# Kernel optimization log

Hardware: AMD Instinct MI355X
Metric: run time of the kernel (lower is better)

Reference implementation:

```python
import jax, jax.numpy as jnp
import numpy as np

# Config / sizes
N = 20000       # nodes
E = 320000      # edges (avg degree 16)
IN_DIM = 6      # node feature dim
PE = 8          # laplacian PE dims
ED = 4          # edge feature dim
H = 128         # hidden dim
OUT = 4         # output dim
L = 3           # message-passing layers
T = 3           # node types (typed encoders/decoders)


def mlp(z, W1, b1, W2, b2):
    # _make_mlp: Linear -> ReLU -> Linear
    return jax.nn.relu(z @ W1 + b1) @ W2 + b2


def typed_mlp(z, W1, b1, W2, b2, types):
    # W1: [T, Din, H]; compute all T branches, select per-node by type
    h = jax.nn.relu(jnp.einsum('ni,tih->tnh', z, W1) + b1[:, None, :])
    o = jnp.einsum('tnh,tho->tno', h, W2) + b2[:, None, :]
    onehot = jax.nn.one_hot(types, W1.shape[0], dtype=o.dtype)  # [N, T]
    return jnp.einsum('tno,nt->no', o, onehot)


def setup_inputs() -> dict:
    key = jax.random.key(0)
    ks = jax.random.split(key, 40)

    def w(k, shape, fan_in):
        return jax.random.normal(k, shape, dtype=jnp.float32) / np.float32(np.sqrt(fan_in))

    inp = {}
    inp['x'] = jax.random.normal(ks[0], (N, IN_DIM), dtype=jnp.float32)
    inp['pe'] = jax.random.normal(ks[1], (N, PE), dtype=jnp.float32)
    inp['edge_attr'] = jax.random.normal(ks[2], (E, ED), dtype=jnp.float32)
    # typed node encoders: (in_dim+pe_dims) -> H -> H
    inp['enc_W1'] = w(ks[3], (T, IN_DIM + PE, H), IN_DIM + PE)
    inp['enc_b1'] = jnp.zeros((T, H), jnp.float32)
    inp['enc_W2'] = w(ks[4], (T, H, H), H)
    inp['enc_b2'] = jnp.zeros((T, H), jnp.float32)
    # edge encoder: ED -> H -> H
    inp['ee_W1'] = w(ks[5], (ED, H), ED)
    inp['ee_b1'] = jnp.zeros((H,), jnp.float32)
    inp['ee_W2'] = w(ks[6], (H, H), H)
    inp['ee_b2'] = jnp.zeros((H,), jnp.float32)
    # per-layer edge update (3H->H->H), node update (2H->H->H), fusion (H->H->H)
    inp['eu_W1'] = w(ks[7], (L, 3 * H, H), 3 * H)
    inp['eu_b1'] = jnp.zeros((L, H), jnp.float32)
    inp['eu_W2'] = w(ks[8], (L, H, H), H)
    inp['eu_b2'] = jnp.zeros((L, H), jnp.float32)
    inp['nu_W1'] = w(ks[9], (L, 2 * H, H), 2 * H)
    inp['nu_b1'] = jnp.zeros((L, H), jnp.float32)
    inp['nu_W2'] = w(ks[10], (L, H, H), H)
    inp['nu_b2'] = jnp.zeros((L, H), jnp.float32)
    inp['fu_W1'] = w(ks[11], (L, H, H), H)
    inp['fu_b1'] = jnp.zeros((L, H), jnp.float32)
    inp['fu_W2'] = w(ks[12], (L, H, H), H)
    inp['fu_b2'] = jnp.zeros((L, H), jnp.float32)
    # typed decoders: H -> H -> OUT
    inp['dec_W1'] = w(ks[13], (T, H, H), H)
    inp['dec_b1'] = jnp.zeros((T, H), jnp.float32)
    inp['dec_W2'] = w(ks[14], (T, H, OUT), H)
    inp['dec_b2'] = jnp.zeros((T, OUT), jnp.float32)
    # int inputs
    inp['edge_index'] = jax.random.randint(ks[15], (2, E), 0, N)
    inp['node_types'] = jax.random.randint(ks[16], (N,), 0, T)
    return inp


def reference(x, pe, edge_attr,
              enc_W1, enc_b1, enc_W2, enc_b2,
              ee_W1, ee_b1, ee_W2, ee_b2,
              eu_W1, eu_b1, eu_W2, eu_b2,
              nu_W1, nu_b1, nu_W2, nu_b2,
              fu_W1, fu_b1, fu_W2, fu_b2,
              dec_W1, dec_b1, dec_W2, dec_b2,
              edge_index, node_types):
    n = x.shape[0]
    src, dst = edge_index[0], edge_index[1]
    # typed node encode on [x || pe]
    h_nodes = typed_mlp(jnp.concatenate([x, pe], axis=-1),
                        enc_W1, enc_b1, enc_W2, enc_b2, node_types)
    # edge encode
    h_edges = mlp(edge_attr, ee_W1, ee_b1, ee_W2, ee_b2)
    num_layers = eu_W1.shape[0]
    for l in range(num_layers):
        # gather endpoint states, edge MLP, residual on edges
        m_edge = mlp(jnp.concatenate([h_nodes[src], h_nodes[dst], h_edges], axis=-1),
                     eu_W1[l], eu_b1[l], eu_W2[l], eu_b2[l])
        h_edges = h_edges + m_edge
        # scatter-add aggregation to destination nodes (index_add_)
        m_node = jax.ops.segment_sum(h_edges, dst, num_segments=n)
        # node update + residual, then fusion (dropout is eval/identity)
        upd = mlp(jnp.concatenate([h_nodes, m_node], axis=-1),
                  nu_W1[l], nu_b1[l], nu_W2[l], nu_b2[l])
        local = h_nodes + upd
        h_nodes = mlp(local, fu_W1[l], fu_b1[l], fu_W2[l], fu_b2[l])
    # typed decode
    out = typed_mlp(h_nodes, dec_W1, dec_b1, dec_W2, dec_b2, node_types)
    return out
```

## Files before the change

### kernel.cpp

```cpp
#include <hip/hip_runtime.h>
#include <hip/hip_bf16.h>

typedef __hip_bfloat16 bf16;
typedef __attribute__((ext_vector_type(8))) short short8;
typedef __attribute__((ext_vector_type(4))) float floatx4;

#define HDIM 128
#define NCANON 27

__device__ __forceinline__ float b2f(bf16 v) { return __bfloat162float(v); }
__device__ __forceinline__ float s2f(short s) {
  return __uint_as_float(((unsigned int)(unsigned short)s) << 16);
}
__device__ __forceinline__ short f2s(float f) {
  return (short)__bfloat16_as_ushort(__float2bfloat16(f));
}

struct CanonDesc {
  const void* src[NCANON];
  int prefix[NCANON + 1];
};

__global__ void canon_kernel(CanonDesc d, const unsigned short* __restrict__ xraw,
                             int* __restrict__ flagOut, bf16* __restrict__ out, int total,
// ... 79 lines not shown
  }
}

__global__ void scan1_kernel(const int* __restrict__ cnt, int* __restrict__ bsum, int n) {
  int tid = threadIdx.x, lane = tid & 63, wave = tid >> 6;
  int i = blockIdx.x * 256 + tid;
  int v = (i < n) ? cnt[i] : 0;
  #pragma unroll
  for (int d = 32; d; d >>= 1) v += __shfl_down(v, d);
  __shared__ int ws[4];
  if (lane == 0) ws[wave] = v;
  __syncthreads();
  if (tid == 0) bsum[blockIdx.x] = ws[0] + ws[1] + ws[2] + ws[3];
}

__global__ void scan2_kernel(int* __restrict__ bsum, int nb) {
  int lane = threadIdx.x;
  int a0 = (lane < nb) ? bsum[lane] : 0;
  int b0 = (64 + lane < nb) ? bsum[64 + lane] : 0;
  int a = a0, b = b0;
  #pragma unroll
  for (int d = 1; d < 64; d <<= 1) { int t = __shfl_up(a, d); if (lane >= d) a += t; }
  int totA = __shfl(a, 63);
  #pragma unroll
  for (int d = 1; d < 64; d <<= 1) { int t = __shfl_up(b, d); if (lane >= d) b += t; }
  int totB = __shfl(b, 63);
  if (lane < nb) bsum[lane] = a - a0;
  if (64 + lane < nb) bsum[64 + lane] = b - b0 + totA;
  if (lane == 0) bsum[nb] = totA + totB;
}

__global__ void scan3_kernel(const int* __restrict__ cnt, const int* __restrict__ bsum,
                             int* __restrict__ row_start, int n, int nb) {
  __shared__ int sh[256];
  int tid = threadIdx.x;
  int i = blockIdx.x * 256 + tid;
  int v = (i < n) ? cnt[i] : 0;
  sh[tid] = v;
  __syncthreads();
  #pragma unroll
  for (int off = 1; off < 256; off <<= 1) {
    int t = (tid >= off) ? sh[tid - off] : 0;
    __syncthreads();
    sh[tid] += t;
    __syncthreads();
  }
  if (i < n) row_start[i] = bsum[blockIdx.x] + sh[tid] - v;
  if (blockIdx.x == 0 && tid == 0) row_start[n] = bsum[nb];
}

__global__ void scatter_kernel(const int* __restrict__ src, const int* __restrict__ dst,
                               const int* __restrict__ row_start, int* __restrict__ cursor,
                               const bf16* __restrict__ ea, bf16* __restrict__ eaS,
                               int* __restrict__ srcS, int* __restrict__ dstS, int E) {
  int e = blockIdx.x * 256 + threadIdx.x;
  if (e < E) {
    int d = dst[e];
    int pos = row_start[d] + atomicAdd(&cursor[d], 1);
    srcS[pos] = src[e];
    dstS[pos] = d;
    *(uint2*)(eaS + (size_t)pos * 4) = *(const uint2*)(ea + (size_t)e * 4);
  }
}

struct PackJob { const bf16* src; bf16* dst; int Ksrc; int KS; int srcCols; };
struct PackJobs { PackJob j[40]; };

__global__ void pack_all_kernel(PackJobs J) {
  PackJob job = J.j[blockIdx.y];
  int idx = blockIdx.x * 256 + threadIdx.x;
  int total = 8 * job.KS * 64;
  if (idx >= total) return;
  int lane = idx & 63;
  int ks = (idx >> 6) % job.KS;
  int ct = idx / (64 * job.KS);
  bf16* o = job.dst + (size_t)idx * 8;
  int ncol = ct * 16 + (lane & 15);
  int kb = ks * 32 + ((lane >> 4) & 3) * 8;
  #pragma unroll
  for (int jj = 0; jj < 8; jj++) {
    int k = kb + jj;
    o[jj] = (k < job.Ksrc && ncol < job.srcCols)
              ? job.src[(size_t)k * job.srcCols + ncol] : __float2bfloat16(0.f);
  }
}

__global__ void __launch_bounds__(256) ygemm_kernel(
    const bf16* __restrict__ X,
    const bf16* __restrict__ WpA, const bf16* __restrict__ WpB,
    bf16* __restrict__ outA, bf16* __restrict__ outB,
    float* __restrict__ mnode, int M) {
  const bf16* Wp = blockIdx.y ? WpB : WpA;
  bf16* outp = blockIdx.y ? outB : outA;
  constexpr int BM = 64, RT = 4, SK = 144;
  __shared__ bf16 Zt[BM * SK];
  const int tid = threadIdx.x;
  const int lane = tid & 63, wave = tid >> 6, colq = lane & 15, quad = lane >> 4;
  const int row0 = blockIdx.x * BM;
  if (blockIdx.y == 0) {
    float4 z = {0.f, 0.f, 0.f, 0.f};
    for (int i = tid; i < BM * 32; i += 256) {
      int row = i >> 5, q = i & 31;
      int gr = row0 + row;
      if (gr < M) *(float4*)(mnode + (size_t)gr * HDIM + q * 4) = z;
    }
  }
  {
    int row = tid >> 2, sub = tid & 3;
    int gr = row0 + row;
    bool ok = gr < M;
    #pragma unroll
    for (int j = 0; j < 4; j++) {
      int seg = j * 4 + sub;
      uint4 v = {0u, 0u, 0u, 0u};
      if (ok) v = *(const uint4*)(X + (size_t)gr * HDIM + seg * 8);
      *(uint4*)(&Zt[row * SK + seg * 8]) = v;
    }
  }
  __syncthreads();
  floatx4 acc[RT][2];
  #pragma unroll
  for (int rt = 0; rt < RT; rt++)
    #pragma unroll
    for (int c = 0; c < 2; c++) acc[rt][c] = (floatx4){0.f, 0.f, 0.f, 0.f};
  #pragma unroll
  for (int ks = 0; ks < 4; ks++) {
    short8 bfr0 = *(const short8*)(Wp + (((size_t)(wave * 2 + 0) * 4 + ks) * 64 + lane) * 8);
    short8 bfr1 = *(const short8*)(Wp + (((size_t)(wave * 2 + 1) * 4 + ks) * 64 + lane) * 8);
    #pragma unroll
    for (int rt = 0; rt < RT; rt++) {
      short8 a = *(const short8*)(&Zt[(rt * 16 + colq) * SK + ks * 32 + quad * 8]);
      acc[rt][0] = __builtin_amdgcn_mfma_f32_16x16x32_bf16(a, bfr0, acc[rt][0], 0, 0, 0);
      acc[rt][1] = __builtin_amdgcn_mfma_f32_16x16x32_bf16(a, bfr1, acc[rt][1], 0, 0, 0);
    }
  }
  __syncthreads();
  #pragma unroll
  for (int c = 0; c < 2; c++) {
    int col = wave * 32 + c * 16 + colq;
    #pragma unroll
    for (int rt = 0; rt < RT; rt++)
      #pragma unroll
      for (int r = 0; r < 4; r++)
        Zt[(rt * 16 + quad * 4 + r) * SK + col] = __float2bfloat16(acc[rt][c][r]);
  }
  __syncthreads();
  for (int i = tid; i < BM * 16; i += 256) {
    int row = i >> 4, seg = i & 15;
    int gr = row0 + row;
    if (gr < M)
      *(uint4*)(outp + (size_t)gr * HDIM + seg * 8) = *(const uint4*)(&Zt[row * SK + seg * 8]);
  }
}

template<bool WRITE_HE>
__global__ void __launch_bounds__(512) eu_kernel(
    const bf16* __restrict__ he, const bf16* __restrict__ ysrc, const bf16* __restrict__ ydst,
    const int* __restrict__ srcS, const int* __restrict__ dstS,
    const bf16* __restrict__ W1p, const bf16* __restrict__ b1v,
    const bf16* __restrict__ W2p, const bf16* __restrict__ b2v,
    bf16* __restrict__ outp, float* __restrict__ mnode, int M) {
  constexpr int BM = 64, RT = 4, SK = 272;
  __shared__ bf16 Zt[BM * SK];
  __shared__ int dstLds[BM];
  const int tid = threadIdx.x;
  const int lane = tid & 63, wave = tid >> 6, colq = lane & 15, quad = lane >> 4;
  const int nwg = gridDim.x, bid = blockIdx.x;
  const int qq = nwg >> 3, rr = nwg & 7;
  const int xcd = bid & 7, bidx = bid >> 3;
  const int blk = (xcd < rr ? xcd * (qq + 1) : rr * (qq + 1) + (xcd - rr) * qq) + bidx;
  const int row0 = blk * BM;
  {
    int row = tid >> 3, sub = tid & 7;
    int gr = row0 + row;
    bool ok = gr < M;
    int g0 = ok ? srcS[gr] : 0;
    int g1 = ok ? dstS[gr] : 0;
    if (sub == 0) dstLds[row] = ok ? g1 : -1;
    #pragma unroll
    for (int j = 0; j < 4; j++) {
      int c = j * 8 + sub;
      int part = c >> 4, seg = c & 15;
      if (part == 0) {
        short8 o = {0, 0, 0, 0, 0, 0, 0, 0};
        if (ok) {
          short8 a = *(const short8*)(ysrc + (size_t)g0 * HDIM + seg * 8);
          short8 b = *(const short8*)(ydst + (size_t)g1 * HDIM + seg * 8);
          #pragma unroll
          for (int k = 0; k < 8; k++) o[k] = f2s(s2f(a[k]) + s2f(b[k]));
        }
        *(short8*)(&Zt[row * SK + seg * 8]) = o;
      } else {
        uint4 v = {0u, 0u, 0u, 0u};
        if (ok) v = *(const uint4*)(he + (size_t)gr * HDIM + seg * 8);
        *(uint4*)(&Zt[row * SK + 128 + seg * 8]) = v;
      }
    }
  }
  __syncthreads();

  floatx4 acc[RT];
  #pragma unroll
  for (int rt = 0; rt < RT; rt++) acc[rt] = (floatx4){0.f, 0.f, 0.f, 0.f};
  #pragma unroll
  for (int ks = 0; ks < 4; ks++) {
    short8 bfr = *(const short8*)(W1p + (((size_t)wave * 4 + ks) * 64 + lane) * 8);
    #pragma unroll
    for (int rt = 0; rt < RT; rt++) {
      short8 a = *(const short8*)(&Zt[(rt * 16 + colq) * SK + 128 + ks * 32 + quad * 8]);
      acc[rt] = __builtin_amdgcn_mfma_f32_16x16x32_bf16(a, bfr, acc[rt], 0, 0, 0);
    }
  }
  {
    int col = wave * 16 + colq;
    float bv = b2f(b1v[col]);
    #pragma unroll
    for (int rt = 0; rt < RT; rt++)
      #pragma unroll
      for (int r = 0; r < 4; r++) {
        int lrow = rt * 16 + quad * 4 + r;
        float v = acc[rt][r] + bv + b2f(Zt[lrow * SK + col]);
        Zt[lrow * SK + col] = __float2bfloat16(fmaxf(v, 0.f));
      }
  }
  __syncthreads();

  #pragma unroll
  for (int rt = 0; rt < RT; rt++) acc[rt] = (floatx4){0.f, 0.f, 0.f, 0.f};
  #pragma unroll
  for (int ks = 0; ks < 4; ks++) {
    short8 bfr = *(const short8*)(W2p + (((size_t)wave * 4 + ks) * 64 + lane) * 8);
    #pragma unroll
    for (int rt = 0; rt < RT; rt++) {
      short8 a = *(const short8*)(&Zt[(rt * 16 + colq) * SK + ks * 32 + quad * 8]);
// ... 171 lines not shown
      #pragma unroll
      for (int r = 0; r < 4; r++)
        Zt[(wr * 32 + rt * 16 + quad * 4 + r) * SK + 128 + col] =
            __float2bfloat16(fmaxf(acc[rt][c][r] + bv, 0.f));
  }
  __syncthreads();

  #pragma unroll
  for (int rt = 0; rt < 2; rt++)
    #pragma unroll
    for (int c = 0; c < 2; c++) acc[rt][c] = (floatx4){0.f, 0.f, 0.f, 0.f};
  #pragma unroll
  for (int ks = 0; ks < 4; ks++) {
    short8 bfr0 = *(const short8*)(fuW2 + (((size_t)(wc * 2 + 0) * 4 + ks) * 64 + lane) * 8);
    short8 bfr1 = *(const short8*)(fuW2 + (((size_t)(wc * 2 + 1) * 4 + ks) * 64 + lane) * 8);
    #pragma unroll
    for (int rt = 0; rt < 2; rt++) {
      short8 a = *(const short8*)(&Zt[(wr * 32 + rt * 16 + colq) * SK + 128 + ks * 32 + quad * 8]);
      acc[rt][0] = __builtin_amdgcn_mfma_f32_16x16x32_bf16(a, bfr0, acc[rt][0], 0, 0, 0);
      acc[rt][1] = __builtin_amdgcn_mfma_f32_16x16x32_bf16(a, bfr1, acc[rt][1], 0, 0, 0);
    }
  }
  #pragma unroll
  for (int c = 0; c < 2; c++) {
    int col = wc * 32 + c * 16 + colq;
    float bv = b2f(fuB2[col]);
    #pragma unroll
    for (int rt = 0; rt < 2; rt++)
      #pragma unroll
      for (int r = 0; r < 4; r++) {
        int lrow = wr * 32 + rt * 16 + quad * 4 + r;
        Zt[lrow * SK + col] = __float2bfloat16(acc[rt][c][r] + bv);
      }
  }
  __syncthreads();
  for (int i = tid; i < BM * 16; i += 512) {
    int row = i >> 4, seg = i & 15;
    int gr = row0 + row;
    if (gr < M)
      *(uint4*)(outp + (size_t)gr * HDIM + seg * 8) = *(const uint4*)(&Zt[row * SK + seg * 8]);
  }
  if (!yW1a) return;

  #pragma unroll
  for (int which = 0; which < 2; which++) {
    const bf16* Wp = which ? yW1b : yW1a;
    bf16* outy = which ? ysB : ysA;
    #pragma unroll
    for (int rt = 0; rt < 2; rt++)
      #pragma unroll
      for (int c = 0; c < 2; c++) acc[rt][c] = (floatx4){0.f, 0.f, 0.f, 0.f};
    #pragma unroll
    for (int ks = 0; ks < 4; ks++) {
      short8 bfr0 = *(const short8*)(Wp + (((size_t)(wc * 2 + 0) * 4 + ks) * 64 + lane) * 8);
      short8 bfr1 = *(const short8*)(Wp + (((size_t)(wc * 2 + 1) * 4 + ks) * 64 + lane) * 8);
      #pragma unroll
      for (int rt = 0; rt < 2; rt++) {
        short8 a = *(const short8*)(&Zt[(wr * 32 + rt * 16 + colq) * SK + ks * 32 + quad * 8]);
        acc[rt][0] = __builtin_amdgcn_mfma_f32_16x16x32_bf16(a, bfr0, acc[rt][0], 0, 0, 0);
        acc[rt][1] = __builtin_amdgcn_mfma_f32_16x16x32_bf16(a, bfr1, acc[rt][1], 0, 0, 0);
      }
    }
    #pragma unroll
    for (int c = 0; c < 2; c++) {
      int col = wc * 32 + c * 16 + colq;
      #pragma unroll
      for (int rt = 0; rt < 2; rt++)
        #pragma unroll
        for (int r = 0; r < 4; r++)
          Zt[(wr * 32 + rt * 16 + quad * 4 + r) * SK + 128 + col] =
              __float2bfloat16(acc[rt][c][r]);
    }
    __syncthreads();
    for (int i = tid; i < BM * 16; i += 512) {
      int row = i >> 4, seg = i & 15;
      int gr = row0 + row;
      if (gr < M)
        *(uint4*)(outy + (size_t)gr * HDIM + seg * 8) = *(const uint4*)(&Zt[row * SK + 128 + seg * 8]);
    }
    __syncthreads();
  }
}

__global__ void __launch_bounds__(256) encee_kernel(
    int eeBlocks, int ngrid64,
    const bf16* __restrict__ eaS,
    const bf16* __restrict__ eeW1, const bf16* __restrict__ eeB1,
    const bf16* __restrict__ eeW2, const bf16* __restrict__ eeB2,
    bf16* __restrict__ h_edges, int E,
    const bf16* __restrict__ x, const bf16* __restrict__ pe,
    const int* __restrict__ perm, const int* __restrict__ ts,
    const bf16* __restrict__ encW1, const bf16* __restrict__ encB1,
    const bf16* __restrict__ encW2, const bf16* __restrict__ encB2,
    bf16* __restrict__ h_nodes) {
  __shared__ bf16 smem[128 * 144];
  __shared__ int gIdx[64];
  const int tid = threadIdx.x;
  const int lane = tid & 63, wave = tid >> 6, colq = lane & 15, quad = lane >> 4;

  if (blockIdx.x < eeBlocks) {
    constexpr int BM = 128, RT = 8, SK = 144;
    bf16* Zt = smem;
    const int row0 = blockIdx.x * BM;
    for (int i = tid; i < BM * 4; i += 256) {
      int row = i >> 2, seg = i & 3;
      int gr = row0 + row;
      uint4 val = {0u, 0u, 0u, 0u};
      if (seg == 0 && gr < E) {
        uint2 v = *(const uint2*)(eaS + (size_t)gr * 4);
        val.x = v.x; val.y = v.y;
      }
      *(uint4*)(&Zt[row * SK + seg * 8]) = val;
    }
    __syncthreads();
    floatx4 acc[RT][2];
    #pragma unroll
    for (int rt = 0; rt < RT; rt++)
      #pragma unroll
      for (int c = 0; c < 2; c++) acc[rt][c] = (floatx4){0.f, 0.f, 0.f, 0.f};
    {
      short8 bfr0 = *(const short8*)(eeW1 + (((size_t)(wave * 2 + 0)) * 64 + lane) * 8);
      short8 bfr1 = *(const short8*)(eeW1 + (((size_t)(wave * 2 + 1)) * 64 + lane) * 8);
      #pragma unroll
      for (int rt = 0; rt < RT; rt++) {
        short8 a = *(const short8*)(&Zt[(rt * 16 + colq) * SK + quad * 8]);
        acc[rt][0] = __builtin_amdgcn_mfma_f32_16x16x32_bf16(a, bfr0, acc[rt][0], 0, 0, 0);
        acc[rt][1] = __builtin_amdgcn_mfma_f32_16x16x32_bf16(a, bfr1, acc[rt][1], 0, 0, 0);
      }
    }
    __syncthreads();
    #pragma unroll
    for (int c = 0; c < 2; c++) {
      int col = wave * 32 + c * 16 + colq;
      float bv = b2f(eeB1[col]);
      #pragma unroll
      for (int rt = 0; rt < RT; rt++)
        #pragma unroll
        for (int r = 0; r < 4; r++)
          Zt[(rt * 16 + quad * 4 + r) * SK + col] =
              __float2bfloat16(fmaxf(acc[rt][c][r] + bv, 0.f));
    }
    __syncthreads();
    floatx4 acc2[RT][2];
    #pragma unroll
    for (int rt = 0; rt < RT; rt++)
      #pragma unroll
      for (int c = 0; c < 2; c++) acc2[rt][c] = (floatx4){0.f, 0.f, 0.f, 0.f};
    #pragma unroll
    for (int ks = 0; ks < 4; ks++) {
      short8 bfr0 = *(const short8*)(eeW2 + (((size_t)(wave * 2 + 0) * 4 + ks) * 64 + lane) * 8);
      short8 bfr1 = *(const short8*)(eeW2 + (((size_t)(wave * 2 + 1) * 4 + ks) * 64 + lane) * 8);
      #pragma unroll
      for (int rt = 0; rt < RT; rt++) {
        short8 a = *(const short8*)(&Zt[(rt * 16 + colq) * SK + ks * 32 + quad * 8]);
        acc2[rt][0] = __builtin_amdgcn_mfma_f32_16x16x32_bf16(a, bfr0, acc2[rt][0], 0, 0, 0);
        acc2[rt][1] = __builtin_amdgcn_mfma_f32_16x16x32_bf16(a, bfr1, acc2[rt][1], 0, 0, 0);
      }
    }
    __syncthreads();
    #pragma unroll
    for (int c = 0; c < 2; c++) {
      int col = wave * 32 + c * 16 + colq;
      float bv = b2f(eeB2[col]);
      #pragma unroll
      for (int rt = 0; rt < RT; rt++)
        #pragma unroll
        for (int r = 0; r < 4; r++)
          Zt[(rt * 16 + quad * 4 + r) * SK + col] = __float2bfloat16(acc2[rt][c][r] + bv);
    }
    __syncthreads();
    for (int i = tid; i < BM * 16; i += 256) {
      int row = i >> 4, seg = i & 15;
      int gr = row0 + row;
      if (gr < E)
        *(uint4*)(h_edges + (size_t)gr * HDIM + seg * 8) = *(const uint4*)(&Zt[row * SK + seg * 8]);
    }
    return;
  }

  {
    constexpr int BM = 64, RT = 4, SK = 40, HS = 144;
    bf16* Zt = smem;
    bf16* Hid = smem + BM * SK;
    int idx = blockIdx.x - eeBlocks;
    int t = idx / ngrid64;
    int bx = idx - t * ngrid64;
    int rs = ts[t], re = ts[t + 1];
    int row0 = rs + bx * BM;
    if (row0 >= re) return;
    for (int i = tid; i < BM; i += 256) gIdx[i] = (row0 + i < re) ? perm[row0 + i] : -1;
    __syncthreads();
    for (int i = tid; i < BM * 32; i += 256) {
      int row = i >> 5, k = i & 31;
      int g = gIdx[row];
      bf16 v = __float2bfloat16(0.f);
      if (g >= 0 && k < 14) v = (k < 6) ? x[(size_t)g * 6 + k] : pe[(size_t)g * 8 + (k - 6)];
      Zt[row * SK + k] = v;
    }
    __syncthreads();
    const bf16* W1t = encW1 + (size_t)t * 4096;
    const bf16* W2t = encW2 + (size_t)t * 16384;
    floatx4 acc[RT][2];
    #pragma unroll
    for (int rt = 0; rt < RT; rt++)
      #pragma unroll
      for (int c = 0; c < 2; c++) acc[rt][c] = (floatx4){0.f, 0.f, 0.f, 0.f};
    {
      short8 bfr0 = *(const short8*)(W1t + (((size_t)(wave * 2 + 0)) * 64 + lane) * 8);
      short8 bfr1 = *(const short8*)(W1t + (((size_t)(wave * 2 + 1)) * 64 + lane) * 8);
      #pragma unroll
      for (int rt = 0; rt < RT; rt++) {
        short8 a = *(const short8*)(&Zt[(rt * 16 + colq) * SK + quad * 8]);
        acc[rt][0] = __builtin_amdgcn_mfma_f32_16x16x32_bf16(a, bfr0, acc[rt][0], 0, 0, 0);
        acc[rt][1] = __builtin_amdgcn_mfma_f32_16x16x32_bf16(a, bfr1, acc[rt][1], 0, 0, 0);
      }
    }
    #pragma unroll
    for (int c = 0; c < 2; c++) {
      int col = wave * 32 + c * 16 + colq;
      float bv = b2f(encB1[t * HDIM + col]);
      #pragma unroll
      for (int rt = 0; rt < RT; rt++)
        #pragma unroll
        for (int r = 0; r < 4; r++)
          Hid[(rt * 16 + quad * 4 + r) * HS + col] =
              __float2bfloat16(fmaxf(acc[rt][c][r] + bv, 0.f));
    }
    __syncthreads();
    floatx4 acc2[RT][2];
    #pragma unroll
    for (int rt = 0; rt < RT; rt++)
      #pragma unroll
      for (int c = 0; c < 2; c++) acc2[rt][c] = (floatx4){0.f, 0.f, 0.f, 0.f};
    #pragma unroll
    for (int ks = 0; ks < 4; ks++) {
      short8 bfr0 = *(const short8*)(W2t + (((size_t)(wave * 2 + 0) * 4 + ks) * 64 + lane) * 8);
      short8 bfr1 = *(const short8*)(W2t + (((size_t)(wave * 2 + 1) * 4 + ks) * 64 + lane) * 8);
      #pragma unroll
      for (int rt = 0; rt < RT; rt++) {
        short8 a = *(const short8*)(&Hid[(rt * 16 + colq) * HS + ks * 32 + quad * 8]);
        acc2[rt][0] = __builtin_amdgcn_mfma_f32_16x16x32_bf16(a, bfr0, acc2[rt][0], 0, 0, 0);
        acc2[rt][1] = __builtin_amdgcn_mfma_f32_16x16x32_bf16(a, bfr1, acc2[rt][1], 0, 0, 0);
      }
    }
    #pragma unroll
    for (int c = 0; c < 2; c++) {
      int col = wave * 32 + c * 16 + colq;
      float bv = b2f(encB2[t * HDIM + col]);
      #pragma unroll
      for (int rt = 0; rt < RT; rt++)
        #pragma unroll
        for (int r = 0; r < 4; r++) {
          int g = gIdx[rt * 16 + quad * 4 + r];
          if (g >= 0) h_nodes[(size_t)g * HDIM + col] = __float2bfloat16(acc2[rt][c][r] + bv);
        }
    }
  }
}

__global__ void __launch_bounds__(256) dec_kernel(
    const bf16* __restrict__ in0,
    const int* __restrict__ perm, const int* __restrict__ ts, const int* __restrict__ flagp,
    const bf16* __restrict__ W1p, const bf16* __restrict__ b1v,
    const bf16* __restrict__ W2p, const bf16* __restrict__ b2v,
    void* __restrict__ outp) {
  constexpr int BM = 64, RT = 4, SK = 144, HS = 144;
  int t = blockIdx.y;
  int rs = ts[t], re = ts[t + 1];
  int row0 = rs + blockIdx.x * BM;
  if (row0 >= re) return;
  __shared__ bf16 Zt[BM * SK];
  __shared__ bf16 Hid[BM * HS];
  __shared__ int gIdx[BM];
  const int tid = threadIdx.x;
  const int lane = tid & 63, wave = tid >> 6, colq = lane & 15, quad = lane >> 4;
  for (int i = tid; i < BM; i += 256) gIdx[i] = (row0 + i < re) ? perm[row0 + i] : -1;
  __syncthreads();
  {
    int row = tid >> 2, sub = tid & 3;
    int g = gIdx[row];
    #pragma unroll
    for (int j = 0; j < 4; j++) {
      int seg = j * 4 + sub;
      uint4 v = {0u, 0u, 0u, 0u};
      if (g >= 0) v = *(const uint4*)(in0 + (size_t)g * HDIM + seg * 8);
      *(uint4*)(&Zt[row * SK + seg * 8]) = v;
    }
  }
  __syncthreads();
  const bf16* W1t = W1p + (size_t)t * 16384;
  const bf16* W2t = W2p + (size_t)t * 16384;
  floatx4 acc[RT][2];
  #pragma unroll
  for (int rt = 0; rt < RT; rt++)
    #pragma unroll
    for (int c = 0; c < 2; c++) acc[rt][c] = (floatx4){0.f, 0.f, 0.f, 0.f};
  #pragma unroll
  for (int ks = 0; ks < 4; ks++) {
    short8 bfr0 = *(const short8*)(W1t + (((size_t)(wave * 2 + 0) * 4 + ks) * 64 + lane) * 8);
    short8 bfr1 = *(const short8*)(W1t + (((size_t)(wave * 2 + 1) * 4 + ks) * 64 + lane) * 8);
    #pragma unroll
    for (int rt = 0; rt < RT; rt++) {
      short8 a = *(const short8*)(&Zt[(rt * 16 + colq) * SK + ks * 32 + quad * 8]);
      acc[rt][0] = __builtin_amdgcn_mfma_f32_16x16x32_bf16(a, bfr0, acc[rt][0], 0, 0, 0);
      acc[rt][1] = __builtin_amdgcn_mfma_f32_16x16x32_bf16(a, bfr1, acc[rt][1], 0, 0, 0);
    }
  }
  #pragma unroll
  for (int c = 0; c < 2; c++) {
    int col = wave * 32 + c * 16 + colq;
    float bv = b2f(b1v[t * HDIM + col]);
    #pragma unroll
    for (int rt = 0; rt < RT; rt++)
      #pragma unroll
      for (int r = 0; r < 4; r++)
        Hid[(rt * 16 + quad * 4 + r) * HS + col] =
            __float2bfloat16(fmaxf(acc[rt][c][r] + bv, 0.f));
  }
  __syncthreads();
  floatx4 acc2[RT];
  #pragma unroll
  for (int rt = 0; rt < RT; rt++) acc2[rt] = (floatx4){0.f, 0.f, 0.f, 0.f};
  #pragma unroll
  for (int ks = 0; ks < 4; ks++) {
    short8 bfr0 = *(const short8*)(W2t + (((size_t)0 * 4 + ks) * 64 + lane) * 8);
    #pragma unroll
    for (int rt = 0; rt < RT; rt++) {
      short8 a = *(const short8*)(&Hid[(rt * 16 + colq) * HS + ks * 32 + quad * 8]);
      acc2[rt] = __builtin_amdgcn_mfma_f32_16x16x32_bf16(a, bfr0, acc2[rt], 0, 0, 0);
    }
  }
  if (wave == 0 && colq < 4) {
    int isBf = flagp[0];
    float bv = b2f(b2v[t * 4 + colq]);
    #pragma unroll
    for (int rt = 0; rt < RT; rt++)
      #pragma unroll
      for (int r = 0; r < 4; r++) {
        int g = gIdx[rt * 16 + quad * 4 + r];
        if (g >= 0) {
          float v = acc2[rt][r] + bv;
          if (isBf) ((bf16*)outp)[(size_t)g * 4 + colq] = __float2bfloat16(v);
          else      ((float*)outp)[(size_t)g * 4 + colq] = v;
        }
      }
  }
}

extern "C" void kernel_launch(void* const* d_in, const int* in_sizes, int n_in,
                              void* d_out, int out_size, void* d_ws, size_t ws_size,
                              hipStream_t stream) {
  const int* edge_index = (const int*)d_in[27];
  const int* node_types = (const int*)d_in[28];
  const int N = in_sizes[28];
  const int E = in_sizes[2] / 4;
  const int L = in_sizes[12] / HDIM;
  const int* srcI = edge_index;
  const int* dstI = edge_index + E;

  CanonDesc cd;
  int total = 0;
  for (int i = 0; i < NCANON; i++) { cd.src[i] = d_in[i]; cd.prefix[i] = total; total += in_sizes[i]; }
  cd.prefix[NCANON] = total;

  char* wsb = (char*)d_ws;
  size_t off = 0;
  auto alloc = [&](size_t bytes) -> void* {
    void* p = wsb + off;
    off += (bytes + 255) & ~(size_t)255;
    return p;
  };
  int*  flag      = (int*)alloc(256);
  bf16* arena     = (bf16*)alloc((size_t)total * 2);
  bf16* h_nodes   = (bf16*)alloc((size_t)N * HDIM * 2);
  bf16* h_edges   = (bf16*)alloc((size_t)E * HDIM * 2);
  float* m_node   = (float*)alloc((size_t)N * HDIM * 4);
  bf16* ysrcb     = (bf16*)alloc((size_t)N * HDIM * 2);
  bf16* ydstb     = (bf16*)alloc((size_t)N * HDIM * 2);
  bf16* eaS       = (bf16*)alloc((size_t)E * 4 * 2);
  int* counts     = (int*)alloc((size_t)N * 4);
  int* cursor     = (int*)alloc((size_t)N * 4);
  int* row_start  = (int*)alloc((size_t)(N + 1) * 4);
  int* bsum       = (int*)alloc(260 * 4);
  int* srcS       = (int*)alloc((size_t)E * 4);
  int* dstS       = (int*)alloc((size_t)E * 4);
  int* tsArr      = (int*)alloc(64);
  int* permT      = (int*)alloc((size_t)N * 4);
  bf16* eeW1p  = (bf16*)alloc(4096 * 2);
  bf16* eeW2p  = (bf16*)alloc(16384 * 2);
  bf16* encW1p = (bf16*)alloc(3 * 4096 * 2);
  bf16* encW2p = (bf16*)alloc(3 * 16384 * 2);
  bf16* decW1p = (bf16*)alloc(3 * 16384 * 2);
  bf16* decW2p = (bf16*)alloc(3 * 16384 * 2);
  bf16* euW1a  = (bf16*)alloc((size_t)L * 16384 * 2);
  bf16* euW1b  = (bf16*)alloc((size_t)L * 16384 * 2);
  bf16* euW1c  = (bf16*)alloc((size_t)L * 16384 * 2);
  bf16* euW2p  = (bf16*)alloc((size_t)L * 16384 * 2);
  bf16* nuW1p  = (bf16*)alloc((size_t)L * 32768 * 2);
  bf16* nuW2p  = (bf16*)alloc((size_t)L * 16384 * 2);
  bf16* fuW1p  = (bf16*)alloc((size_t)L * 16384 * 2);
  bf16* fuW2p  = (bf16*)alloc((size_t)L * 16384 * 2);

  const bf16* cX     = arena + cd.prefix[0];
  const bf16* cPE    = arena + cd.prefix[1];
  const bf16* cEA    = arena + cd.prefix[2];
  const bf16* cEncW1 = arena + cd.prefix[3];
  const bf16* cEncB1 = arena + cd.prefix[4];
  const bf16* cEncW2 = arena + cd.prefix[5];
  const bf16* cEncB2 = arena + cd.prefix[6];
  const bf16* cEeW1  = arena + cd.prefix[7];
  const bf16* cEeB1  = arena + cd.prefix[8];
  const bf16* cEeW2  = arena + cd.prefix[9];
  const bf16* cEeB2  = arena + cd.prefix[10];
  const bf16* cEuW1  = arena + cd.prefix[11];
  const bf16* cEuB1  = arena + cd.prefix[12];
  const bf16* cEuW2  = arena + cd.prefix[13];
  const bf16* cEuB2  = arena + cd.prefix[14];
  const bf16* cNuW1  = arena + cd.prefix[15];
  const bf16* cNuB1  = arena + cd.prefix[16];
  const bf16* cNuW2  = arena + cd.prefix[17];
  const bf16* cNuB2  = arena + cd.prefix[18];
  const bf16* cFuW1  = arena + cd.prefix[19];
  const bf16* cFuB1  = arena + cd.prefix[20];
  const bf16* cFuW2  = arena + cd.prefix[21];
  const bf16* cFuB2  = arena + cd.prefix[22];
  const bf16* cDecW1 = arena + cd.prefix[23];
  const bf16* cDecB1 = arena + cd.prefix[24];
  const bf16* cDecW2 = arena + cd.prefix[25];
  const bf16* cDecB2 = arena + cd.prefix[26];

  int canonBlocks = (total + 255) / 256;
  size_t zbytes = (size_t)((char*)cursor - (char*)counts) + (size_t)N * 4;
  int zquads = (int)(zbytes / 16);
  int zBlocks = (zquads + 255) / 256;
  canon_kernel<<<canonBlocks + zBlocks, 256, 0, stream>>>(
      cd, (const unsigned short*)d_in[0], flag, arena, total, canonBlocks,
      (uint4*)counts, zquads);

  int hb = (E + 1023) / 1024;
  hist_tsort_kernel<<<hb + 1, 1024, 0, stream>>>(dstI, counts, E, hb,
                                                 node_types, tsArr, permT, N);

  PackJobs PJ;
  int nj = 0;
  PJ.j[nj++] = {cEeW1, eeW1p, 4, 1, 128};
  PJ.j[nj++] = {cEeW2, eeW2p, 128, 4, 128};
  for (int l = 0; l < L; l++) {
    const bf16* w1 = cEuW1 + (size_t)l * 384 * HDIM;
    PJ.j[nj++] = {w1,                 euW1a + (size_t)l * 16384, 128, 4, 128};
    PJ.j[nj++] = {w1 + 128 * HDIM,    euW1b + (size_t)l * 16384, 128, 4, 128};
    PJ.j[nj++] = {w1 + 256 * HDIM,    euW1c + (size_t)l * 16384, 128, 4, 128};
    PJ.j[nj++] = {cEuW2 + (size_t)l * HDIM * HDIM, euW2p + (size_t)l * 16384, 128, 4, 128};
    PJ.j[nj++] = {cNuW1 + (size_t)l * 256 * HDIM,  nuW1p + (size_t)l * 32768, 256, 8, 128};
    PJ.j[nj++] = {cNuW2 + (size_t)l * HDIM * HDIM, nuW2p + (size_t)l * 16384, 128, 4, 128};
    PJ.j[nj++] = {cFuW1 + (size_t)l * HDIM * HDIM, fuW1p + (size_t)l * 16384, 128, 4, 128};
    PJ.j[nj++] = {cFuW2 + (size_t)l * HDIM * HDIM, fuW2p + (size_t)l * 16384, 128, 4, 128};
  }
  for (int t = 0; t < 3; t++) {
    PJ.j[nj++] = {cEncW1 + (size_t)t * 14 * HDIM,   encW1p + (size_t)t * 4096, 14, 1, 128};
    PJ.j[nj++] = {cEncW2 + (size_t)t * HDIM * HDIM, encW2p + (size_t)t * 16384, 128, 4, 128};
    PJ.j[nj++] = {cDecW1 + (size_t)t * HDIM * HDIM, decW1p + (size_t)t * 16384, 128, 4, 128};
    PJ.j[nj++] = {cDecW2 + (size_t)t * HDIM * 4,    decW2p + (size_t)t * 16384, 128, 4, 4};
  }
  pack_all_kernel<<<dim3(16, nj), 256, 0, stream>>>(PJ);

  int nb = (N + 255) / 256;
  scan1_kernel<<<nb, 256, 0, stream>>>(counts, bsum, N);
  scan2_kernel<<<1, 64, 0, stream>>>(bsum, nb);
  scan3_kernel<<<nb, 256, 0, stream>>>(counts, bsum, row_start, N, nb);
  scatter_kernel<<<(E + 255) / 256, 256, 0, stream>>>(srcI, dstI, row_start, cursor,
                                                      cEA, eaS, srcS, dstS, E);

  int ngrid64  = (N + 63) / 64;
  int egrid64  = (E + 63) / 64;
  int egrid128 = (E + 127) / 128;

  encee_kernel<<<egrid128 + 3 * ngrid64, 256, 0, stream>>>(
      egrid128, ngrid64,
      eaS, eeW1p, cEeB1, eeW2p, cEeB2, h_edges, E,
      cX, cPE, permT, tsArr, encW1p, cEncB1, encW2p, cEncB2, h_nodes);

  for (int l = 0; l < L; l++) {
    if (l == 0) {
      ygemm_kernel<<<dim3(ngrid64, 2), 256, 0, stream>>>(
          h_nodes, euW1a, euW1b, ysrcb, ydstb, m_node, N);
    }
    if (l + 1 < L) {
      eu_kernel<true><<<egrid64, 512, 0, stream>>>(
          h_edges, ysrcb, ydstb, srcS, dstS,
          euW1c + (size_t)l * 16384, cEuB1 + l * HDIM,
          euW2p + (size_t)l * 16384, cEuB2 + l * HDIM, h_edges, m_node, E);
    } else {
      eu_kernel<false><<<egrid64, 512, 0, stream>>>(
          h_edges, ysrcb, ydstb, srcS, dstS,
          euW1c + (size_t)l * 16384, cEuB1 + l * HDIM,
          euW2p + (size_t)l * 16384, cEuB2 + l * HDIM, h_edges, m_node, E);
    }
    bool hasNext = (l + 1 < L);
    node_kernel<<<ngrid64, 512, 0, stream>>>(
        h_nodes, m_node,
        nuW1p + (size_t)l * 32768, cNuB1 + l * HDIM,
        nuW2p + (size_t)l * 16384, cNuB2 + l * HDIM,
        fuW1p + (size_t)l * 16384, cFuB1 + l * HDIM,
        fuW2p + (size_t)l * 16384, cFuB2 + l * HDIM,
        hasNext ? euW1a + (size_t)(l + 1) * 16384 : nullptr,
        hasNext ? euW1b + (size_t)(l + 1) * 16384 : nullptr,
        ysrcb, ydstb, h_nodes, N);
  }

  dec_kernel<<<dim3(ngrid64, 3), 256, 0, stream>>>(
      h_nodes, permT, tsArr, flag, decW1p, cDecB1, decW2p, cDecB2, d_out);
  (void)n_in; (void)ws_size;
}
```

Baseline: 448.2 us.

## Fuse layer-0 endpoint projections into encoder kernel and zero m_node in canon

Removes the separate ygemm kernel. The layer-0 source and destination projections of the node states are now computed inside the typed node encoder, reusing the encoded tile already held in shared memory. Zeroing of m_node moves into the existing zero-fill pass of the canon kernel by reordering allocations so the buffer is contiguous with counts and cursor. The encoder kernel grows to 512 threads with a 2x4 wave layout, which saves one launch and one read of h_nodes but adds register and shared-memory pressure and more work per encoder block.

```diff
diff --git a/kernel.cpp b/kernel.cpp
--- a/kernel.cpp
+++ b/kernel.cpp
@@ -185,74 +185,6 @@
     int k = kb + jj;
     o[jj] = (k < job.Ksrc && ncol < job.srcCols)
               ? job.src[(size_t)k * job.srcCols + ncol] : __float2bfloat16(0.f);
-  }
-}
-
-__global__ void __launch_bounds__(256) ygemm_kernel(
-    const bf16* __restrict__ X,
-    const bf16* __restrict__ WpA, const bf16* __restrict__ WpB,
-    bf16* __restrict__ outA, bf16* __restrict__ outB,
-    float* __restrict__ mnode, int M) {
-  const bf16* Wp = blockIdx.y ? WpB : WpA;
-  bf16* outp = blockIdx.y ? outB : outA;
-  constexpr int BM = 64, RT = 4, SK = 144;
-  __shared__ bf16 Zt[BM * SK];
-  const int tid = threadIdx.x;
-  const int lane = tid & 63, wave = tid >> 6, colq = lane & 15, quad = lane >> 4;
-  const int row0 = blockIdx.x * BM;
-  if (blockIdx.y == 0) {
-    float4 z = {0.f, 0.f, 0.f, 0.f};
-    for (int i = tid; i < BM * 32; i += 256) {
-      int row = i >> 5, q = i & 31;
-      int gr = row0 + row;
-      if (gr < M) *(float4*)(mnode + (size_t)gr * HDIM + q * 4) = z;
-    }
-  }
-  {
-    int row = tid >> 2, sub = tid & 3;
-    int gr = row0 + row;
-    bool ok = gr < M;
-    #pragma unroll
-    for (int j = 0; j < 4; j++) {
-      int seg = j * 4 + sub;
-      uint4 v = {0u, 0u, 0u, 0u};
-      if (ok) v = *(const uint4*)(X + (size_t)gr * HDIM + seg * 8);
-      *(uint4*)(&Zt[row * SK + seg * 8]) = v;
-    }
-  }
-  __syncthreads();
-  floatx4 acc[RT][2];
-  #pragma unroll
-  for (int rt = 0; rt < RT; rt++)
-    #pragma unroll
-    for (int c = 0; c < 2; c++) acc[rt][c] = (floatx4){0.f, 0.f, 0.f, 0.f};
-  #pragma unroll
-  for (int ks = 0; ks < 4; ks++) {
-    short8 bfr0 = *(const short8*)(Wp + (((size_t)(wave * 2 + 0) * 4 + ks) * 64 + lane) * 8);
-    short8 bfr1 = *(const short8*)(Wp + (((size_t)(wave * 2 + 1) * 4 + ks) * 64 + lane) * 8);
-    #pragma unroll
-    for (int rt = 0; rt < RT; rt++) {
-      short8 a = *(const short8*)(&Zt[(rt * 16 + colq) * SK + ks * 32 + quad * 8]);
-      acc[rt][0] = __builtin_amdgcn_mfma_f32_16x16x32_bf16(a, bfr0, acc[rt][0], 0, 0, 0);
-      acc[rt][1] = __builtin_amdgcn_mfma_f32_16x16x32_bf16(a, bfr1, acc[rt][1], 0, 0, 0);
-    }
-  }
-  __syncthreads();
-  #pragma unroll
-  for (int c = 0; c < 2; c++) {
-    int col = wave * 32 + c * 16 + colq;
-    #pragma unroll
-    for (int rt = 0; rt < RT; rt++)
-      #pragma unroll
-      for (int r = 0; r < 4; r++)
-        Zt[(rt * 16 + quad * 4 + r) * SK + col] = __float2bfloat16(acc[rt][c][r]);
-  }
-  __syncthreads();
-  for (int i = tid; i < BM * 16; i += 256) {
-    int row = i >> 4, seg = i & 15;
-    int gr = row0 + row;
-    if (gr < M)
-      *(uint4*)(outp + (size_t)gr * HDIM + seg * 8) = *(const uint4*)(&Zt[row * SK + seg * 8]);
   }
 }
 
@@ -590,7 +522,7 @@
   }
 }
 
-__global__ void __launch_bounds__(256) encee_kernel(
+__global__ void __launch_bounds__(512) encee_kernel(
     int eeBlocks, int ngrid64,
     const bf16* __restrict__ eaS,
     const bf16* __restrict__ eeW1, const bf16* __restrict__ eeB1,
@@ -600,17 +532,21 @@
     const int* __restrict__ perm, const int* __restrict__ ts,
     const bf16* __restrict__ encW1, const bf16* __restrict__ encB1,
     const bf16* __restrict__ encW2, const bf16* __restrict__ encB2,
-    bf16* __restrict__ h_nodes) {
+    bf16* __restrict__ h_nodes,
+    const bf16* __restrict__ yW1a, const bf16* __restrict__ yW1b,
+    bf16* __restrict__ ysA, bf16* __restrict__ ysB) {
   __shared__ bf16 smem[128 * 144];
   __shared__ int gIdx[64];
   const int tid = threadIdx.x;
   const int lane = tid & 63, wave = tid >> 6, colq = lane & 15, quad = lane >> 4;
+  const int wr = wave >> 2, wc = wave & 3;
 
   if (blockIdx.x < eeBlocks) {
-    constexpr int BM = 128, RT = 8, SK = 144;
+    constexpr int BM = 128, RT = 4, SK = 144;
     bf16* Zt = smem;
     const int row0 = blockIdx.x * BM;
-    for (int i = tid; i < BM * 4; i += 256) {
+    {
+      int i = tid;
       int row = i >> 2, seg = i & 3;
       int gr = row0 + row;
       uint4 val = {0u, 0u, 0u, 0u};
@@ -627,11 +563,11 @@
       #pragma unroll
       for (int c = 0; c < 2; c++) acc[rt][c] = (floatx4){0.f, 0.f, 0.f, 0.f};
     {
-      short8 bfr0 = *(const short8*)(eeW1 + (((size_t)(wave * 2 + 0)) * 64 + lane) * 8);
-      short8 bfr1 = *(const short8*)(eeW1 + (((size_t)(wave * 2 + 1)) * 64 + lane) * 8);
+      short8 bfr0 = *(const short8*)(eeW1 + (((size_t)(wc * 2 + 0)) * 64 + lane) * 8);
+      short8 bfr1 = *(const short8*)(eeW1 + (((size_t)(wc * 2 + 1)) * 64 + lane) * 8);
       #pragma unroll
       for (int rt = 0; rt < RT; rt++) {
-        short8 a = *(const short8*)(&Zt[(rt * 16 + colq) * SK + quad * 8]);
+        short8 a = *(const short8*)(&Zt[(wr * 64 + rt * 16 + colq) * SK + quad * 8]);
         acc[rt][0] = __builtin_amdgcn_mfma_f32_16x16x32_bf16(a, bfr0, acc[rt][0], 0, 0, 0);
         acc[rt][1] = __builtin_amdgcn_mfma_f32_16x16x32_bf16(a, bfr1, acc[rt][1], 0, 0, 0);
       }
@@ -639,13 +575,13 @@
     __syncthreads();
     #pragma unroll
     for (int c = 0; c < 2; c++) {
-      int col = wave * 32 + c * 16 + colq;
+      int col = wc * 32 + c * 16 + colq;
       float bv = b2f(eeB1[col]);
       #pragma unroll
       for (int rt = 0; rt < RT; rt++)
         #pragma unroll
         for (int r = 0; r < 4; r++)
-          Zt[(rt * 16 + quad * 4 + r) * SK + col] =
+          Zt[(wr * 64 + rt * 16 + quad * 4 + r) * SK + col] =
               __float2bfloat16(fmaxf(acc[rt][c][r] + bv, 0.f));
     }
     __syncthreads();
@@ -656,11 +592,11 @@
       for (int c = 0; c < 2; c++) acc2[rt][c] = (floatx4){0.f, 0.f, 0.f, 0.f};
     #pragma unroll
     for (int ks = 0; ks < 4; ks++) {
-      short8 bfr0 = *(const short8*)(eeW2 + (((size_t)(wave * 2 + 0) * 4 + ks) * 64 + lane) * 8);
-      short8 bfr1 = *(const short8*)(eeW2 + (((size_t)(wave * 2 + 1) * 4 + ks) * 64 + lane) * 8);
+      short8 bfr0 = *(const short8*)(eeW2 + (((size_t)(wc * 2 + 0) * 4 + ks) * 64 + lane) * 8);
+      short8 bfr1 = *(const short8*)(eeW2 + (((size_t)(wc * 2 + 1) * 4 + ks) * 64 + lane) * 8);
       #pragma unroll
       for (int rt = 0; rt < RT; rt++) {
-        short8 a = *(const short8*)(&Zt[(rt * 16 + colq) * SK + ks * 32 + quad * 8]);
+        short8 a = *(const short8*)(&Zt[(wr * 64 + rt * 16 + colq) * SK + ks * 32 + quad * 8]);
         acc2[rt][0] = __builtin_amdgcn_mfma_f32_16x16x32_bf16(a, bfr0, acc2[rt][0], 0, 0, 0);
         acc2[rt][1] = __builtin_amdgcn_mfma_f32_16x16x32_bf16(a, bfr1, acc2[rt][1], 0, 0, 0);
       }
@@ -668,16 +604,17 @@
     __syncthreads();
     #pragma unroll
     for (int c = 0; c < 2; c++) {
-      int col = wave * 32 + c * 16 + colq;
+      int col = wc * 32 + c * 16 + colq;
       float bv = b2f(eeB2[col]);
       #pragma unroll
       for (int rt = 0; rt < RT; rt++)
         #pragma unroll
         for (int r = 0; r < 4; r++)
-          Zt[(rt * 16 + quad * 4 + r) * SK + col] = __float2bfloat16(acc2[rt][c][r] + bv);
-    }
-    __syncthreads();
-    for (int i = tid; i < BM * 16; i += 256) {
+          Zt[(wr * 64 + rt * 16 + quad * 4 + r) * SK + col] =
+              __float2bfloat16(acc2[rt][c][r] + bv);
+    }
+    __syncthreads();
+    for (int i = tid; i < BM * 16; i += 512) {
       int row = i >> 4, seg = i & 15;
       int gr = row0 + row;
       if (gr < E)
@@ -687,81 +624,119 @@
   }
 
   {
-    constexpr int BM = 64, RT = 4, SK = 40, HS = 144;
+    constexpr int BM = 64, SKz = 40, HS = 144;
     bf16* Zt = smem;
-    bf16* Hid = smem + BM * SK;
+    bf16* Hid = smem + BM * SKz;
     int idx = blockIdx.x - eeBlocks;
     int t = idx / ngrid64;
     int bx = idx - t * ngrid64;
     int rs = ts[t], re = ts[t + 1];
     int row0 = rs + bx * BM;
     if (row0 >= re) return;
-    for (int i = tid; i < BM; i += 256) gIdx[i] = (row0 + i < re) ? perm[row0 + i] : -1;
-    __syncthreads();
-    for (int i = tid; i < BM * 32; i += 256) {
+    for (int i = tid; i < BM; i += 512) gIdx[i] = (row0 + i < re) ? perm[row0 + i] : -1;
+    __syncthreads();
+    for (int i = tid; i < BM * 32; i += 512) {
       int row = i >> 5, k = i & 31;
       int g = gIdx[row];
       bf16 v = __float2bfloat16(0.f);
       if (g >= 0 && k < 14) v = (k < 6) ? x[(size_t)g * 6 + k] : pe[(size_t)g * 8 + (k - 6)];
-      Zt[row * SK + k] = v;
+      Zt[row * SKz + k] = v;
     }
     __syncthreads();
     const bf16* W1t = encW1 + (size_t)t * 4096;
     const bf16* W2t = encW2 + (size_t)t * 16384;
-    floatx4 acc[RT][2];
-    #pragma unroll
-    for (int rt = 0; rt < RT; rt++)
+    floatx4 acc[2][2];
+    #pragma unroll
+    for (int rt = 0; rt < 2; rt++)
       #pragma unroll
       for (int c = 0; c < 2; c++) acc[rt][c] = (floatx4){0.f, 0.f, 0.f, 0.f};
     {
-      short8 bfr0 = *(const short8*)(W1t + (((size_t)(wave * 2 + 0)) * 64 + lane) * 8);
-      short8 bfr1 = *(const short8*)(W1t + (((size_t)(wave * 2 + 1)) * 64 + lane) * 8);
-      #pragma unroll
-      for (int rt = 0; rt < RT; rt++) {
-        short8 a = *(const short8*)(&Zt[(rt * 16 + colq) * SK + quad * 8]);
+      short8 bfr0 = *(const short8*)(W1t + (((size_t)(wc * 2 + 0)) * 64 + lane) * 8);
+      short8 bfr1 = *(const short8*)(W1t + (((size_t)(wc * 2 + 1)) * 64 + lane) * 8);
+      #pragma unroll
+      for (int rt = 0; rt < 2; rt++) {
+        short8 a = *(const short8*)(&Zt[(wr * 32 + rt * 16 + colq) * SKz + quad * 8]);
         acc[rt][0] = __builtin_amdgcn_mfma_f32_16x16x32_bf16(a, bfr0, acc[rt][0], 0, 0, 0);
         acc[rt][1] = __builtin_amdgcn_mfma_f32_16x16x32_bf16(a, bfr1, acc[rt][1], 0, 0, 0);
       }
     }
     #pragma unroll
     for (int c = 0; c < 2; c++) {
-      int col = wave * 32 + c * 16 + colq;
+      int col = wc * 32 + c * 16 + colq;
       float bv = b2f(encB1[t * HDIM + col]);
       #pragma unroll
-      for (int rt = 0; rt < RT; rt++)
+      for (int rt = 0; rt < 2; rt++)
         #pragma unroll
         for (int r = 0; r < 4; r++)
-          Hid[(rt * 16 + quad * 4 + r) * HS + col] =
+          Hid[(wr * 32 + rt * 16 + quad * 4 + r) * HS + col] =
               __float2bfloat16(fmaxf(acc[rt][c][r] + bv, 0.f));
     }
     __syncthreads();
-    floatx4 acc2[RT][2];
-    #pragma unroll
-    for (int rt = 0; rt < RT; rt++)
+    floatx4 acc2[2][2];
+    #pragma unroll
+    for (int rt = 0; rt < 2; rt++)
       #pragma unroll
       for (int c = 0; c < 2; c++) acc2[rt][c] = (floatx4){0.f, 0.f, 0.f, 0.f};
     #pragma unroll
     for (int ks = 0; ks < 4; ks++) {
-      short8 bfr0 = *(const short8*)(W2t + (((size_t)(wave * 2 + 0) * 4 + ks) * 64 + lane) * 8);
-      short8 bfr1 = *(const short8*)(W2t + (((size_t)(wave * 2 + 1) * 4 + ks) * 64 + lane) * 8);
-      #pragma unroll
-      for (int rt = 0; rt < RT; rt++) {
-        short8 a = *(const short8*)(&Hid[(rt * 16 + colq) * HS + ks * 32 + quad * 8]);
+      short8 bfr0 = *(const short8*)(W2t + (((size_t)(wc * 2 + 0) * 4 + ks) * 64 + lane) * 8);
+      short8 bfr1 = *(const short8*)(W2t + (((size_t)(wc * 2 + 1) * 4 + ks) * 64 + lane) * 8);
+      #pragma unroll
+      for (int rt = 0; rt < 2; rt++) {
+        short8 a = *(const short8*)(&Hid[(wr * 32 + rt * 16 + colq) * HS + ks * 32 + quad * 8]);
         acc2[rt][0] = __builtin_amdgcn_mfma_f32_16x16x32_bf16(a, bfr0, acc2[rt][0], 0, 0, 0);
         acc2[rt][1] = __builtin_amdgcn_mfma_f32_16x16x32_bf16(a, bfr1, acc2[rt][1], 0, 0, 0);
       }
     }
+    __syncthreads();
     #pragma unroll
     for (int c = 0; c < 2; c++) {
-      int col = wave * 32 + c * 16 + colq;
+      int col = wc * 32 + c * 16 + colq;
       float bv = b2f(encB2[t * HDIM + col]);
       #pragma unroll
-      for (int rt = 0; rt < RT; rt++)
+      for (int rt = 0; rt < 2; rt++)
         #pragma unroll
         for (int r = 0; r < 4; r++) {
-          int g = gIdx[rt * 16 + quad * 4 + r];
-          if (g >= 0) h_nodes[(size_t)g * HDIM + col] = __float2bfloat16(acc2[rt][c][r] + bv);
+          int row = wr * 32 + rt * 16 + quad * 4 + r;
+          int g = gIdx[row];
+          bf16 hb = __float2bfloat16(acc2[rt][c][r] + bv);
+          Hid[row * HS + col] = hb;
+          if (g >= 0) h_nodes[(size_t)g * HDIM + col] = hb;
         }
+    }
+    __syncthreads();
+
+    #pragma unroll
+    for (int which = 0; which < 2; which++) {
+      const bf16* Wp = which ? yW1b : yW1a;
+      bf16* outy = which ? ysB : ysA;
+      floatx4 accy[2][2];
+      #pragma unroll
+      for (int rt = 0; rt < 2; rt++)
+        #pragma unroll
+        for (int c = 0; c < 2; c++) accy[rt][c] = (floatx4){0.f, 0.f, 0.f, 0.f};
+      #pragma unroll
+      for (int ks = 0; ks < 4; ks++) {
+        short8 bfr0 = *(const short8*)(Wp + (((size_t)(wc * 2 + 0) * 4 + ks) * 64 + lane) * 8);
+        short8 bfr1 = *(const short8*)(Wp + (((size_t)(wc * 2 + 1) * 4 + ks) * 64 + lane) * 8);
+        #pragma unroll
+        for (int rt = 0; rt < 2; rt++) {
+          short8 a = *(const short8*)(&Hid[(wr * 32 + rt * 16 + colq) * HS + ks * 32 + quad * 8]);
+          accy[rt][0] = __builtin_amdgcn_mfma_f32_16x16x32_bf16(a, bfr0, accy[rt][0], 0, 0, 0);
+          accy[rt][1] = __builtin_amdgcn_mfma_f32_16x16x32_bf16(a, bfr1, accy[rt][1], 0, 0, 0);
+        }
+      }
+      #pragma unroll
+      for (int c = 0; c < 2; c++) {
+        int col = wc * 32 + c * 16 + colq;
+        #pragma unroll
+        for (int rt = 0; rt < 2; rt++)
+          #pragma unroll
+          for (int r = 0; r < 4; r++) {
+            int g = gIdx[wr * 32 + rt * 16 + quad * 4 + r];
+            if (g >= 0) outy[(size_t)g * HDIM + col] = __float2bfloat16(accy[rt][c][r]);
+          }
+      }
     }
   }
 }
@@ -882,10 +857,10 @@
   bf16* arena     = (bf16*)alloc((size_t)total * 2);
   bf16* h_nodes   = (bf16*)alloc((size_t)N * HDIM * 2);
   bf16* h_edges   = (bf16*)alloc((size_t)E * HDIM * 2);
-  float* m_node   = (float*)alloc((size_t)N * HDIM * 4);
   bf16* ysrcb     = (bf16*)alloc((size_t)N * HDIM * 2);
   bf16* ydstb     = (bf16*)alloc((size_t)N * HDIM * 2);
   bf16* eaS       = (bf16*)alloc((size_t)E * 4 * 2);
+  float* m_node   = (float*)alloc((size_t)N * HDIM * 4);
   int* counts     = (int*)alloc((size_t)N * 4);
   int* cursor     = (int*)alloc((size_t)N * 4);
   int* row_start  = (int*)alloc((size_t)(N + 1) * 4);
@@ -938,12 +913,12 @@
   const bf16* cDecB2 = arena + cd.prefix[26];
 
   int canonBlocks = (total + 255) / 256;
-  size_t zbytes = (size_t)((char*)cursor - (char*)counts) + (size_t)N * 4;
+  size_t zbytes = (size_t)((char*)cursor - (char*)m_node) + (size_t)N * 4;
   int zquads = (int)(zbytes / 16);
   int zBlocks = (zquads + 255) / 256;
   canon_kernel<<<canonBlocks + zBlocks, 256, 0, stream>>>(
       cd, (const unsigned short*)d_in[0], flag, arena, total, canonBlocks,
-      (uint4*)counts, zquads);
+      (uint4*)m_node, zquads);
 
   int hb = (E + 1023) / 1024;
   hist_tsort_kernel<<<hb + 1, 1024, 0, stream>>>(dstI, counts, E, hb,
@@ -983,16 +958,13 @@
   int egrid64  = (E + 63) / 64;
   int egrid128 = (E + 127) / 128;
 
-  encee_kernel<<<egrid128 + 3 * ngrid64, 256, 0, stream>>>(
+  encee_kernel<<<egrid128 + 3 * ngrid64, 512, 0, stream>>>(
       egrid128, ngrid64,
       eaS, eeW1p, cEeB1, eeW2p, cEeB2, h_edges, E,
-      cX, cPE, permT, tsArr, encW1p, cEncB1, encW2p, cEncB2, h_nodes);
+      cX, cPE, permT, tsArr, encW1p, cEncB1, encW2p, cEncB2, h_nodes,
+      euW1a, euW1b, ysrcb, ydstb);
 
   for (int l = 0; l < L; l++) {
-    if (l == 0) {
-      ygemm_kernel<<<dim3(ngrid64, 2), 256, 0, stream>>>(
-          h_nodes, euW1a, euW1b, ysrcb, ydstb, m_node, N);
-    }
     if (l + 1 < L) {
       eu_kernel<true><<<egrid64, 512, 0, stream>>>(
           h_edges, ysrcb, ydstb, srcS, dstS,
```

Result: no change. 452.1 us (+0.9%).
